# Performance work log

Measured on AMD Instinct MI355X. Metric: run time of the kernel, lower is better.

The kernel has to match this reference:

```python
import jax, jax.numpy as jnp
import numpy as np
from jax import lax

# CRF hyperparameters (init_kwargs)
MAX_ITER = 10
POS_W, POS_X_STD, POS_Y_STD = 3.0, 3.0, 3.0
BI_W, BI_X_STD, BI_Y_STD = 10.0, 80.0, 80.0
BI_R_STD, BI_G_STD, BI_B_STD = 13.0, 13.0, 13.0


def setup_inputs() -> dict:
    key = jax.random.key(0)
    k1, k2 = jax.random.split(key)
    U = jax.random.normal(k1, (1, 21, 96, 96), dtype=jnp.float32)      # unary energies
    I = jax.random.uniform(k2, (1, 3, 96, 96), dtype=jnp.float32) * 255.0  # RGB image 0..255
    return {"U": U, "I": I}


def _gauss1d(std):
    r = int(3.0 * std)
    x = jnp.arange(-r, r + 1, dtype=jnp.float32)
    return jnp.exp(-0.5 * (x / std) ** 2), r


def _spatial_raw(x, ky, kx, ry, rx):
    # x: [M, 1, H, W]; unnormalized separable Gaussian filter
    x = lax.conv_general_dilated(x, ky.reshape(1, 1, -1, 1), (1, 1), [(ry, ry), (0, 0)],
                                 dimension_numbers=("NCHW", "OIHW", "NCHW"))
    x = lax.conv_general_dilated(x, kx.reshape(1, 1, 1, -1), (1, 1), [(0, 0), (rx, rx)],
                                 dimension_numbers=("NCHW", "OIHW", "NCHW"))
    return x


def reference(U, I):
    B, L, H, W = U.shape
    N = H * W
    ky, ry = _gauss1d(POS_Y_STD)
    kx, rx = _gauss1d(POS_X_STD)

    # symmetric normalization for the spatial kernel: 1/sqrt(k * 1)
    nsp = lax.rsqrt(_spatial_raw(jnp.ones((1, 1, H, W), jnp.float32), ky, kx, ry, rx))  # [1,1,H,W]

    # bilateral kernel K[b, i, j] = exp(-0.5 ||f_i - f_j||^2) over 5-d features
    yy, xx = jnp.meshgrid(jnp.arange(H, dtype=jnp.float32), jnp.arange(W, dtype=jnp.float32), indexing="ij")
    pos = jnp.stack([xx.ravel() / BI_X_STD, yy.ravel() / BI_Y_STD], axis=-1)  # [N, 2]
    rgb_std = jnp.array([BI_R_STD, BI_G_STD, BI_B_STD], jnp.float32)
    col = I.reshape(B, 3, N).transpose(0, 2, 1) / rgb_std                     # [B, N, 3]
    feats = jnp.concatenate([jnp.broadcast_to(pos[None], (B, N, 2)), col], axis=-1)  # [B, N, 5]
    sq = jnp.sum(feats * feats, axis=-1)                                      # [B, N]
    D = sq[:, :, None] + sq[:, None, :] - 2.0 * jnp.einsum("bnf,bmf->bnm", feats, feats)
    K = jnp.exp(-0.5 * jnp.maximum(D, 0.0))                                   # [B, N, N]
    nbi = lax.rsqrt(jnp.sum(K, axis=-1, keepdims=True))                       # [B, N, 1]

    Q0 = jax.nn.softmax(-U, axis=1)

    def step(Q, _):
        Qf = Q.reshape(B * L, 1, H, W)
        sp_msg = POS_W * (nsp * _spatial_raw(nsp * Qf, ky, kx, ry, rx)).reshape(B, L, H, W)
        Qflat = Q.transpose(0, 2, 3, 1).reshape(B, N, L)
        bi = nbi * jnp.einsum("bnm,bml->bnl", K, nbi * Qflat)
        bi_msg = BI_W * bi.reshape(B, H, W, L).transpose(0, 3, 1, 2)
        # Potts compatibility (negative identity): agreeing mass raises the logit
        Qn = jax.nn.softmax(-U + sp_msg + bi_msg, axis=1)
        return Qn, None

    Q, _ = lax.scan(step, Q0, None, length=MAX_ITER)
    return Q
```

## Files before the change

### kernel.cpp

```cpp
#include <hip/hip_runtime.h>
#include <hip/hip_bf16.h>
#include <stddef.h>

#define HH 96
#define WW 96
#define NPIX 9216
#define LBL 21
#define LPAD 32
#define RAD 9
#define N_ITER 10
#define POS_W_C 3.0f
#define BI_W_C 10.0f
#define INV_XY (1.0f/80.0f)
#define INV_RGB (1.0f/13.0f)

#define JCH 12
#define JC (NPIX / JCH)
#define JTOT (NPIX / 32)
#define ROWB (JC * 2 + 16)
#define CHROW (ROWB / 16)
#define TOTCH (32 * CHROW)
#define ITILE 128
#define NITB (NPIX / ITILE)
#define NSPB (LBL * 24)

typedef __bf16 bf16x8 __attribute__((ext_vector_type(8)));
typedef float  f32x4  __attribute__((ext_vector_type(4)));

__device__ const float GK[2 * RAD + 1] = {
    0.01110900f, 0.02856548f, 0.06572886f, 0.13533528f, 0.24935220f,
    0.41111229f, 0.60653066f, 0.80073740f, 0.94595947f, 1.00000000f,
    0.94595947f, 0.80073740f, 0.60653066f, 0.41111229f, 0.24935220f,
    0.13533528f, 0.06572886f, 0.02856548f, 0.01110900f
};

__device__ __forceinline__ unsigned short f2bf(float f) {
    unsigned u = __float_as_uint(f);
    unsigned r = (u + 0x7fffu + ((u >> 16) & 1u)) >> 16;
    return (unsigned short)r;
}
__device__ __forceinline__ float bf2f(unsigned short s) {
    return __uint_as_float(((unsigned)s) << 16);
}
__device__ __forceinline__ unsigned pk2bf(float a, float b) {
    __hip_bfloat162 h = __float22bfloat162_rn(make_float2(a, b));
    return *(unsigned*)&h;
}

__global__ void k_prep(const float* __restrict__ I,
                       float* __restrict__ fx, float* __restrict__ fy,
                       float* __restrict__ fr, float* __restrict__ fg,
                       float* __restrict__ fb, float* __restrict__ S,
                       float* __restrict__ nsp) {
    int n = blockIdx.x * 256 + threadIdx.x;
    if (n >= NPIX) return;
    int y = n / WW, x = n % WW;
    float vx = (float)x * INV_XY;
    float vy = (float)y * INV_XY;
    float vr = I[n] * INV_RGB;
    float vg = I[NPIX + n] * INV_RGB;
    float vb = I[2 * NPIX + n] * INV_RGB;
    fx[n] = vx; fy[n] = vy; fr[n] = vr; fg[n] = vg; fb[n] = vb;
    S[n] = -0.5f * (vx*vx + vy*vy + vr*vr + vg*vg + vb*vb);
    float sy = 0.f, sx = 0.f;
    #pragma unroll
    for (int d = -RAD; d <= RAD; ++d) {
        float g = GK[d + RAD];
        if ((unsigned)(y + d) < HH) sy += g;
        if ((unsigned)(x + d) < WW) sx += g;
    }
    nsp[n] = rsqrtf(sy * sx);
}

template <bool STORE>
__global__ void __launch_bounds__(256)
k_K(const float* __restrict__ fx, const float* __restrict__ fy,
    const float* __restrict__ fr, const float* __restrict__ fg,
    const float* __restrict__ fb, const float* __restrict__ S,
    float* __restrict__ nbi, unsigned short* __restrict__ K) {
    int it = blockIdx.x;
    int tid = threadIdx.x;
    int m = tid & 15;
    int g = tid >> 4;
    int khs = g & 3;
    int ts = g >> 2;
    int i = it * 16 + m;
    float hx = fx[i], hy = fy[i], hr = fr[i], hg = fg[i], hb = fb[i];
    float ci = S[i];
    unsigned short* Kb = K + (size_t)it * JTOT * 512;
    float sum = 0.f;
    for (int pass = 0; pass < JTOT / 4; ++pass) {
        int jtile = pass * 4 + ts;
        int j = jtile * 32 + khs * 8;
        float4 x0 = *(const float4*)(fx + j), x1 = *(const float4*)(fx + j + 4);
        float4 y0 = *(const float4*)(fy + j), y1 = *(const float4*)(fy + j + 4);
        float4 r0 = *(const float4*)(fr + j), r1 = *(const float4*)(fr + j + 4);
        float4 g0 = *(const float4*)(fg + j), g1 = *(const float4*)(fg + j + 4);
        float4 b0 = *(const float4*)(fb + j), b1 = *(const float4*)(fb + j + 4);
        float4 s0 = *(const float4*)(S + j),  s1 = *(const float4*)(S + j + 4);
        float k0 = __expf(ci + s0.x + hx*x0.x + hy*y0.x + hr*r0.x + hg*g0.x + hb*b0.x);
        float k1 = __expf(ci + s0.y + hx*x0.y + hy*y0.y + hr*r0.y + hg*g0.y + hb*b0.y);
        float k2 = __expf(ci + s0.z + hx*x0.z + hy*y0.z + hr*r0.z + hg*g0.z + hb*b0.z);
        float k3 = __expf(ci + s0.w + hx*x0.w + hy*y0.w + hr*r0.w + hg*g0.w + hb*b0.w);
        float k4 = __expf(ci + s1.x + hx*x1.x + hy*y1.x + hr*r1.x + hg*g1.x + hb*b1.x);
        float k5 = __expf(ci + s1.y + hx*x1.y + hy*y1.y + hr*r1.y + hg*g1.y + hb*b1.y);
        float k6 = __expf(ci + s1.z + hx*x1.z + hy*y1.z + hr*r1.z + hg*g1.z + hb*b1.z);
        float k7 = __expf(ci + s1.w + hx*x1.w + hy*y1.w + hr*r1.w + hg*g1.w + hb*b1.w);
        sum += ((k0 + k1) + (k2 + k3)) + ((k4 + k5) + (k6 + k7));
        if (STORE) {
            uint4 u;
            u.x = pk2bf(k0, k1);
            u.y = pk2bf(k2, k3);
            u.z = pk2bf(k4, k5);
            u.w = pk2bf(k6, k7);
            *(uint4*)(Kb + (size_t)jtile * 512 + (tid & 63) * 8) = u;
        }
    }
    __shared__ float red[16][17];
    red[g][m] = sum;
    __syncthreads();
    if (tid < 16) {
        float tot = 0.f;
        #pragma unroll
        for (int q = 0; q < 16; ++q) tot += red[q][tid];
        nbi[it * 16 + tid] = rsqrtf(tot);
    }
}

__global__ void k_q0(const float* __restrict__ U, const float* __restrict__ nbi,
                     const float* __restrict__ nsp, float* __restrict__ A,
                     unsigned short* __restrict__ Qt0, unsigned short* __restrict__ Qt1) {
    int n = blockIdx.x * 256 + threadIdx.x;
    if (n >= NPIX) return;
    float v[LBL];
    float mx = -1e30f;
    #pragma unroll
    for (int l = 0; l < LBL; ++l) { v[l] = -U[l * NPIX + n]; mx = fmaxf(mx, v[l]); }
    float s = 0.f;
    #pragma unroll
    for (int l = 0; l < LBL; ++l) { v[l] = __expf(v[l] - mx); s += v[l]; }
    float inv = 1.f / s;
    float nb = nbi[n];
    float ns = nsp[n];
    #pragma unroll
    for (int l = 0; l < LBL; ++l) {
        float q = v[l] * inv;
        A[l * NPIX + n] = ns * q;
        Qt0[l * NPIX + n] = f2bf(nb * q);
    }
    #pragma unroll
    for (int l = LBL; l < LPAD; ++l) { Qt0[l * NPIX + n] = 0; Qt1[l * NPIX + n] = 0; }
}

__global__ void k_sp(const float* __restrict__ A, const float* __restrict__ nsp,
                     const float* __restrict__ U, float* __restrict__ SP) {
    __shared__ float ty[4 * WW];
    int l = blockIdx.x / 24;
    int y0 = (blockIdx.x % 24) * 4;
    int t = threadIdx.x;
    const float* Al = A + (size_t)l * NPIX;
    #pragma unroll
    for (int c = 0; c < 2; ++c) {
        int p = t + c * 256;
        if (p < 4 * WW) {
            int yy = p / WW, x = p % WW;
            int y = y0 + yy;
            float s = 0.f;
            #pragma unroll
            for (int d = -RAD; d <= RAD; ++d) {
                int yd = y + d;
                if ((unsigned)yd < HH) s += GK[d + RAD] * Al[yd * WW + x];
            }
            ty[p] = s;
        }
    }
    __syncthreads();
    #pragma unroll
    for (int c = 0; c < 2; ++c) {
        int p = t + c * 256;
        if (p < 4 * WW) {
            int yy = p / WW, x = p % WW;
            float s = 0.f;
            #pragma unroll
            for (int d = -RAD; d <= RAD; ++d) {
                int xd = x + d;
                if ((unsigned)xd < WW) s += GK[d + RAD] * ty[yy * WW + xd];
            }
            int pp = (y0 + yy) * WW + x;
            SP[(size_t)l * NPIX + pp] = POS_W_C * nsp[pp] * s - U[(size_t)l * NPIX + pp];
        }
    }
}

__global__ void __launch_bounds__(256)
k_bi_fast(const unsigned short* __restrict__ K, const unsigned short* __restrict__ Qt,
          const float* __restrict__ A, const float* __restrict__ nsp,
          const float* __restrict__ U, float* __restrict__ SP,
          float* __restrict__ P) {
    __shared__ __align__(16) unsigned short Bsh[32 * ROWB / 2];
    int tid = threadIdx.x;
    int bid = blockIdx.x;

    if (bid < NSPB) {
        float* ty = (float*)Bsh;
        int l = bid / 24;
        int y0b = (bid % 24) * 4;
        const float* Al = A + (size_t)l * NPIX;
        #pragma unroll
        for (int c = 0; c < 2; ++c) {
            int p = tid + c * 256;
            if (p < 4 * WW) {
                int yy = p / WW, x = p % WW;
                int y = y0b + yy;
                float s = 0.f;
                #pragma unroll
                for (int d = -RAD; d <= RAD; ++d) {
                    int yd = y + d;
                    if ((unsigned)yd < HH) s += GK[d + RAD] * Al[yd * WW + x];
                }
                ty[p] = s;
            }
        }
        __syncthreads();
        #pragma unroll
        for (int c = 0; c < 2; ++c) {
            int p = tid + c * 256;
            if (p < 4 * WW) {
                int yy = p / WW, x = p % WW;
                float s = 0.f;
                #pragma unroll
                for (int d = -RAD; d <= RAD; ++d) {
                    int xd = x + d;
                    if ((unsigned)xd < WW) s += GK[d + RAD] * ty[yy * WW + xd];
                }
                int pp = (y0b + yy) * WW + x;
                SP[(size_t)l * NPIX + pp] = POS_W_C * nsp[pp] * s - U[(size_t)l * NPIX + pp];
            }
        }
        __syncthreads();
    }

    int jc  = bid / NITB;
    int itb = bid % NITB;
    int base_j = jc * JC;
    int jtb = jc * (JC / 32);

    for (int itn = 0; itn < (TOTCH + 255) / 256; ++itn) {
        int c = itn * 256 + tid;
        if (c < TOTCH) {
            int l = c / CHROW;
            int off = c - l * CHROW;
            int off16 = (off == CHROW - 1) ? 0 : off;
            uint4 v = *(const uint4*)(Qt + (size_t)l * NPIX + base_j + off16 * 8);
            *((uint4*)Bsh + c) = v;
        }
    }
    __syncthreads();

    int lane = tid & 63;
    int wv = tid >> 6;
    int m  = lane & 15;
    int kh = lane >> 4;

    const bf16x8* pa0 = (const bf16x8*)K + ((size_t)(itb * 8 + wv)     * JTOT + jtb) * 64 + lane;
    const bf16x8* pa1 = (const bf16x8*)K + ((size_t)(itb * 8 + 4 + wv) * JTOT + jtb) * 64 + lane;
    const char* lb0 = (const char*)Bsh + m * ROWB + kh * 16;
    const char* lb1 = (const char*)Bsh + (m + 16) * ROWB + kh * 16;

    f32x4 acc00 = {0.f,0.f,0.f,0.f}, acc01 = {0.f,0.f,0.f,0.f};
    f32x4 acc10 = {0.f,0.f,0.f,0.f}, acc11 = {0.f,0.f,0.f,0.f};

    #pragma unroll 4
    for (int jt = 0; jt < JC / 32; ++jt) {
        bf16x8 a0 = pa0[jt * 64];
        bf16x8 a1 = pa1[jt * 64];
        bf16x8 b0 = *(const bf16x8*)(lb0 + jt * 64);
        bf16x8 b1 = *(const bf16x8*)(lb1 + jt * 64);
        acc00 = __builtin_amdgcn_mfma_f32_16x16x32_bf16(a0, b0, acc00, 0, 0, 0);
        acc01 = __builtin_amdgcn_mfma_f32_16x16x32_bf16(a0, b1, acc01, 0, 0, 0);
        acc10 = __builtin_amdgcn_mfma_f32_16x16x32_bf16(a1, b0, acc10, 0, 0, 0);
        acc11 = __builtin_amdgcn_mfma_f32_16x16x32_bf16(a1, b1, acc11, 0, 0, 0);
    }

    float* Pp = P + (size_t)jc * NPIX * 32;
    int i0 = itb * 128 + wv * 16 + kh * 4;
    int i1 = i0 + 64;
    #pragma unroll
    for (int r = 0; r < 4; ++r) {
        Pp[(size_t)(i0 + r) * 32 + m] = acc00[r];
        Pp[(size_t)(i1 + r) * 32 + m] = acc10[r];
        if (m < 8) {
            Pp[(size_t)(i0 + r) * 32 + 16 + m] = acc01[r];
            Pp[(size_t)(i1 + r) * 32 + 16 + m] = acc11[r];
        }
    }
}

__global__ void __launch_bounds__(64)
k_red(const float* __restrict__ P, const float* __restrict__ SP,
      const float* __restrict__ nbi, const float* __restrict__ nsp,
      float* __restrict__ Qo, float* __restrict__ Ao,
      unsigned short* __restrict__ Qto) {
    int lane = threadIdx.x;
    int p = blockIdx.x * 32 + (lane & 31);
    int h = lane >> 5;
    float4 s[6] = {{0,0,0,0},{0,0,0,0},{0,0,0,0},{0,0,0,0},{0,0,0,0},{0,0,0,0}};
    #pragma unroll
    for (int jj = 0; jj < 6; ++jj) {
        int jcc = h * 6 + jj;
        const float4* pp = (const float4*)(P + ((size_t)jcc * NPIX + p) * 32);
        #pragma unroll
        for (int q = 0; q < 6; ++q) s[q] += pp[q];
    }
    float bi[24];
    #pragma unroll
    for (int q = 0; q < 6; ++q) {
        bi[4*q+0] = s[q].x + __shfl_down(s[q].x, 32);
        bi[4*q+1] = s[q].y + __shfl_down(s[q].y, 32);
        bi[4*q+2] = s[q].z + __shfl_down(s[q].z, 32);
        bi[4*q+3] = s[q].w + __shfl_down(s[q].w, 32);
    }
    if (h) return;

    float nb = nbi[p];
    float ns = nsp[p];
    float v[LBL];
    float mx = -1e30f;
    #pragma unroll
    for (int l = 0; l < LBL; ++l) {
        v[l] = SP[l * NPIX + p] + BI_W_C * nb * bi[l];
        mx = fmaxf(mx, v[l]);
    }
    float ssum = 0.f;
    #pragma unroll
    for (int l = 0; l < LBL; ++l) { v[l] = __expf(v[l] - mx); ssum += v[l]; }
    float inv = 1.f / ssum;
    #pragma unroll
    for (int l = 0; l < LBL; ++l) {
        float q = v[l] * inv;
        Qo[l * NPIX + p] = q;
        Ao[l * NPIX + p] = ns * q;
        Qto[l * NPIX + p] = f2bf(nb * q);
    }
}

__global__ void k_bi_slow(const float* __restrict__ fx, const float* __restrict__ fy,
                          const float* __restrict__ fr, const float* __restrict__ fg,
                          const float* __restrict__ fb,
                          const float* __restrict__ nbi, const unsigned short* __restrict__ Qt,
                          const float* __restrict__ SP, const float* __restrict__ nsp,
                          float* __restrict__ Qo, float* __restrict__ Ao,
                          unsigned short* __restrict__ Qto) {
    int t = threadIdx.x;
    int px = t & 15, st = t >> 4;
    int i = blockIdx.x * 16 + px;
    float xi = fx[i], yi = fy[i], ri = fr[i], gi = fg[i], bi = fb[i];
    float acc[LBL];
    #pragma unroll
    for (int l = 0; l < LBL; ++l) acc[l] = 0.f;
    int j0 = st * (NPIX / 16);
    for (int j = j0; j < j0 + NPIX / 16; ++j) {
        float dx = xi - fx[j], dy = yi - fy[j];
        float dr = ri - fr[j], dg = gi - fg[j], db = bi - fb[j];
        float D = dx*dx + dy*dy + dr*dr + dg*dg + db*db;
        float w = __expf(-0.5f * D);
        #pragma unroll
        for (int l = 0; l < LBL; ++l) acc[l] += w * bf2f(Qt[l * NPIX + j]);
    }
    __shared__ float red[16][LBL];
    if (st == 0) {
        #pragma unroll
        for (int l = 0; l < LBL; ++l) red[px][l] = acc[l];
    }
    __syncthreads();
    for (int s = 1; s < 16; ++s) {
        if (st == s) {
            #pragma unroll
            for (int l = 0; l < LBL; ++l) red[px][l] += acc[l];
        }
        __syncthreads();
    }
    if (t < 16) {
        int i2 = blockIdx.x * 16 + t;
        float nb = nbi[i2];
        float ns = nsp[i2];
        float v[LBL];
        float mx = -1e30f;
        #pragma unroll
        for (int l = 0; l < LBL; ++l) {
            v[l] = SP[l * NPIX + i2] + BI_W_C * nb * red[t][l];
            mx = fmaxf(mx, v[l]);
        }
        float s = 0.f;
        #pragma unroll
        for (int l = 0; l < LBL; ++l) { v[l] = __expf(v[l] - mx); s += v[l]; }
        float inv = 1.f / s;
        #pragma unroll
        for (int l = 0; l < LBL; ++l) {
            float q = v[l] * inv;
            Qo[l * NPIX + i2] = q;
            Ao[l * NPIX + i2] = ns * q;
            Qto[l * NPIX + i2] = f2bf(nb * q);
        }
    }
}

extern "C" void kernel_launch(void* const* d_in, const int* in_sizes, int n_in,
                              void* d_out, int out_size, void* d_ws, size_t ws_size,
                              hipStream_t stream) {
    const float* U = (const float*)d_in[0];
    const float* I = (const float*)d_in[1];

    char* w = (char*)d_ws;
    float* fx  = (float*)w;                 w += NPIX * sizeof(float);
    float* fy  = (float*)w;                 w += NPIX * sizeof(float);
    float* fr  = (float*)w;                 w += NPIX * sizeof(float);
    float* fg  = (float*)w;                 w += NPIX * sizeof(float);
    float* fb  = (float*)w;                 w += NPIX * sizeof(float);
    float* S   = (float*)w;                 w += NPIX * sizeof(float);
    float* nsp = (float*)w;                 w += NPIX * sizeof(float);
    float* nbi = (float*)w;                 w += NPIX * sizeof(float);
    float* A   = (float*)w;                 w += (size_t)LBL * NPIX * sizeof(float);
    float* SP  = (float*)w;                 w += (size_t)LBL * NPIX * sizeof(float);
    unsigned short* Qtb[2];
    Qtb[0] = (unsigned short*)w;            w += (size_t)LPAD * NPIX * sizeof(unsigned short);
    Qtb[1] = (unsigned short*)w;            w += (size_t)LPAD * NPIX * sizeof(unsigned short);
    float* P = (float*)w;                   w += (size_t)JCH * NPIX * 32 * sizeof(float);
    unsigned short* K = (unsigned short*)w;
    size_t need = (size_t)(w - (char*)d_ws) + (size_t)NPIX * NPIX * sizeof(unsigned short);
    bool fast = (ws_size >= need);

    float* Qout = (float*)d_out;

    k_prep<<<(NPIX + 255) / 256, 256, 0, stream>>>(I, fx, fy, fr, fg, fb, S, nsp);
    if (fast) k_K<true ><<<NPIX / 16, 256, 0, stream>>>(fx, fy, fr, fg, fb, S, nbi, K);
    else      k_K<false><<<NPIX / 16, 256, 0, stream>>>(fx, fy, fr, fg, fb, S, nbi, nullptr);
    k_q0<<<(NPIX + 255) / 256, 256, 0, stream>>>(U, nbi, nsp, A, Qtb[0], Qtb[1]);

    for (int t = 0; t < N_ITER; ++t) {
        const unsigned short* Qtin = Qtb[t & 1];
        unsigned short* Qtout = Qtb[(t + 1) & 1];
        if (fast) {
            k_bi_fast<<<NITB * JCH, 256, 0, stream>>>(K, Qtin, A, nsp, U, SP, P);
            k_red<<<NPIX / 32, 64, 0, stream>>>(P, SP, nbi, nsp, Qout, A, Qtout);
        } else {
            k_sp<<<NSPB, 256, 0, stream>>>(A, nsp, U, SP);
            k_bi_slow<<<NPIX / 16, 256, 0, stream>>>(fx, fy, fr, fg, fb, nbi, Qtin, SP, nsp, Qout, A, Qtout);
        }
    }
}
```

Before: 554.5 us.

## Split K-matrix build across four blocks per row tile and widen bilateral J split

The bilateral kernel build now launches four blocks per 16-row tile, each covering a quarter of the columns. Partial row sums go to a new RS buffer, and k_q0 finishes the normalization rsqrt. The bilateral matmul split goes from 12 to 16 column chunks, and the partial-product stride shrinks from 32 to 24 floats to cut P traffic. The unroll factor also rises to 6, giving more parallelism in setup and per-iteration kernels at the cost of more partial sums to reduce.

```diff
diff --git a/kernel.cpp b/kernel.cpp
--- a/kernel.cpp
+++ b/kernel.cpp
@@ -14,7 +14,7 @@
 #define INV_XY (1.0f/80.0f)
 #define INV_RGB (1.0f/13.0f)
 
-#define JCH 12
+#define JCH 16
 #define JC (NPIX / JCH)
 #define JTOT (NPIX / 32)
 #define ROWB (JC * 2 + 16)
@@ -23,6 +23,8 @@
 #define ITILE 128
 #define NITB (NPIX / ITILE)
 #define NSPB (LBL * 24)
+#define KSPLIT 4
+#define PSTR 24
 
 typedef __bf16 bf16x8 __attribute__((ext_vector_type(8)));
 typedef float  f32x4  __attribute__((ext_vector_type(4)));
@@ -77,8 +79,9 @@
 k_K(const float* __restrict__ fx, const float* __restrict__ fy,
     const float* __restrict__ fr, const float* __restrict__ fg,
     const float* __restrict__ fb, const float* __restrict__ S,
-    float* __restrict__ nbi, unsigned short* __restrict__ K) {
-    int it = blockIdx.x;
+    float* __restrict__ RS, unsigned short* __restrict__ K) {
+    int it = blockIdx.x >> 2;
+    int part = blockIdx.x & 3;
     int tid = threadIdx.x;
     int m = tid & 15;
     int g = tid >> 4;
@@ -89,8 +92,8 @@
     float ci = S[i];
     unsigned short* Kb = K + (size_t)it * JTOT * 512;
     float sum = 0.f;
-    for (int pass = 0; pass < JTOT / 4; ++pass) {
-        int jtile = pass * 4 + ts;
+    for (int pass = 0; pass < JTOT / (4 * KSPLIT); ++pass) {
+        int jtile = part * (JTOT / KSPLIT) + pass * 4 + ts;
         int j = jtile * 32 + khs * 8;
         float4 x0 = *(const float4*)(fx + j), x1 = *(const float4*)(fx + j + 4);
         float4 y0 = *(const float4*)(fy + j), y1 = *(const float4*)(fy + j + 4);
@@ -123,15 +126,18 @@
         float tot = 0.f;
         #pragma unroll
         for (int q = 0; q < 16; ++q) tot += red[q][tid];
-        nbi[it * 16 + tid] = rsqrtf(tot);
-    }
-}
-
-__global__ void k_q0(const float* __restrict__ U, const float* __restrict__ nbi,
-                     const float* __restrict__ nsp, float* __restrict__ A,
+        RS[part * NPIX + it * 16 + tid] = tot;
+    }
+}
+
+__global__ void k_q0(const float* __restrict__ U, const float* __restrict__ RS,
+                     const float* __restrict__ nsp,
+                     float* __restrict__ nbi, float* __restrict__ A,
                      unsigned short* __restrict__ Qt0, unsigned short* __restrict__ Qt1) {
     int n = blockIdx.x * 256 + threadIdx.x;
     if (n >= NPIX) return;
+    float nb = rsqrtf(RS[n] + RS[NPIX + n] + RS[2 * NPIX + n] + RS[3 * NPIX + n]);
+    nbi[n] = nb;
     float v[LBL];
     float mx = -1e30f;
     #pragma unroll
@@ -140,7 +146,6 @@
     #pragma unroll
     for (int l = 0; l < LBL; ++l) { v[l] = __expf(v[l] - mx); s += v[l]; }
     float inv = 1.f / s;
-    float nb = nbi[n];
     float ns = nsp[n];
     #pragma unroll
     for (int l = 0; l < LBL; ++l) {
@@ -270,7 +275,7 @@
     f32x4 acc00 = {0.f,0.f,0.f,0.f}, acc01 = {0.f,0.f,0.f,0.f};
     f32x4 acc10 = {0.f,0.f,0.f,0.f}, acc11 = {0.f,0.f,0.f,0.f};
 
-    #pragma unroll 4
+    #pragma unroll 6
     for (int jt = 0; jt < JC / 32; ++jt) {
         bf16x8 a0 = pa0[jt * 64];
         bf16x8 a1 = pa1[jt * 64];
@@ -282,16 +287,16 @@
         acc11 = __builtin_amdgcn_mfma_f32_16x16x32_bf16(a1, b1, acc11, 0, 0, 0);
     }
 
-    float* Pp = P + (size_t)jc * NPIX * 32;
+    float* Pp = P + (size_t)jc * NPIX * PSTR;
     int i0 = itb * 128 + wv * 16 + kh * 4;
     int i1 = i0 + 64;
     #pragma unroll
     for (int r = 0; r < 4; ++r) {
-        Pp[(size_t)(i0 + r) * 32 + m] = acc00[r];
-        Pp[(size_t)(i1 + r) * 32 + m] = acc10[r];
+        Pp[(size_t)(i0 + r) * PSTR + m] = acc00[r];
+        Pp[(size_t)(i1 + r) * PSTR + m] = acc10[r];
         if (m < 8) {
-            Pp[(size_t)(i0 + r) * 32 + 16 + m] = acc01[r];
-            Pp[(size_t)(i1 + r) * 32 + 16 + m] = acc11[r];
+            Pp[(size_t)(i0 + r) * PSTR + 16 + m] = acc01[r];
+            Pp[(size_t)(i1 + r) * PSTR + 16 + m] = acc11[r];
         }
     }
 }
@@ -306,9 +311,9 @@
     int h = lane >> 5;
     float4 s[6] = {{0,0,0,0},{0,0,0,0},{0,0,0,0},{0,0,0,0},{0,0,0,0},{0,0,0,0}};
     #pragma unroll
-    for (int jj = 0; jj < 6; ++jj) {
-        int jcc = h * 6 + jj;
-        const float4* pp = (const float4*)(P + ((size_t)jcc * NPIX + p) * 32);
+    for (int jj = 0; jj < JCH / 2; ++jj) {
+        int jcc = h * (JCH / 2) + jj;
+        const float4* pp = (const float4*)(P + ((size_t)jcc * NPIX + p) * PSTR);
         #pragma unroll
         for (int q = 0; q < 6; ++q) s[q] += pp[q];
     }
@@ -420,12 +425,13 @@
     float* S   = (float*)w;                 w += NPIX * sizeof(float);
     float* nsp = (float*)w;                 w += NPIX * sizeof(float);
     float* nbi = (float*)w;                 w += NPIX * sizeof(float);
+    float* RS  = (float*)w;                 w += (size_t)KSPLIT * NPIX * sizeof(float);
     float* A   = (float*)w;                 w += (size_t)LBL * NPIX * sizeof(float);
     float* SP  = (float*)w;                 w += (size_t)LBL * NPIX * sizeof(float);
     unsigned short* Qtb[2];
     Qtb[0] = (unsigned short*)w;            w += (size_t)LPAD * NPIX * sizeof(unsigned short);
     Qtb[1] = (unsigned short*)w;            w += (size_t)LPAD * NPIX * sizeof(unsigned short);
-    float* P = (float*)w;                   w += (size_t)JCH * NPIX * 32 * sizeof(float);
+    float* P = (float*)w;                   w += (size_t)JCH * NPIX * PSTR * sizeof(float);
     unsigned short* K = (unsigned short*)w;
     size_t need = (size_t)(w - (char*)d_ws) + (size_t)NPIX * NPIX * sizeof(unsigned short);
     bool fast = (ws_size >= need);
@@ -433,9 +439,9 @@
     float* Qout = (float*)d_out;
 
     k_prep<<<(NPIX + 255) / 256, 256, 0, stream>>>(I, fx, fy, fr, fg, fb, S, nsp);
-    if (fast) k_K<true ><<<NPIX / 16, 256, 0, stream>>>(fx, fy, fr, fg, fb, S, nbi, K);
-    else      k_K<false><<<NPIX / 16, 256, 0, stream>>>(fx, fy, fr, fg, fb, S, nbi, nullptr);
-    k_q0<<<(NPIX + 255) / 256, 256, 0, stream>>>(U, nbi, nsp, A, Qtb[0], Qtb[1]);
+    if (fast) k_K<true ><<<(NPIX / 16) * KSPLIT, 256, 0, stream>>>(fx, fy, fr, fg, fb, S, RS, K);
+    else      k_K<false><<<(NPIX / 16) * KSPLIT, 256, 0, stream>>>(fx, fy, fr, fg, fb, S, RS, nullptr);
+    k_q0<<<(NPIX + 255) / 256, 256, 0, stream>>>(U, RS, nsp, nbi, A, Qtb[0], Qtb[1]);
 
     for (int t = 0; t < N_ITER; ++t) {
         const unsigned short* Qtin = Qtb[t & 1];
```

Measured after the change: 520.7 us. 6.1% less time.
